# Kernel tuning notes

Hardware: AMD Instinct MI355X
Metric: run time of the kernel (lower is better)

## Reference

```python
import jax, jax.numpy as jnp
import numpy as np
from jax import lax

B, Hs, Ws = 2, 256, 256
DIM = 256        # query channels (c)
DIM_BAK = 256    # key/value channels (c2)
HEADS = 8
WIN = 8
HEAD_DIM = DIM // HEADS
SCALE = HEAD_DIM ** -0.5


def window_partition(x, ws):
    # x: [B, H, W, C] -> [B*nH*nW, ws, ws, C]
    b, h, w, c = x.shape
    x = x.reshape(b, h // ws, ws, w // ws, ws, c)
    return x.transpose(0, 1, 3, 2, 4, 5).reshape(-1, ws, ws, c)


def window_reverse(windows, ws, h, w):
    # windows: [B*nH*nW, ws, ws, C] -> [B, H, W, C]
    b = windows.shape[0] // ((h // ws) * (w // ws))
    x = windows.reshape(b, h // ws, w // ws, ws, ws, -1)
    return x.transpose(0, 1, 3, 2, 4, 5).reshape(b, h, w, -1)


def setup_inputs() -> dict:
    key = jax.random.key(0)
    ks = jax.random.split(key, 9)
    s = 0.02
    return {
        "query_feature": jax.random.normal(ks[0], (B, DIM, Hs, Ws), jnp.float32),
        "key_value_feature": jax.random.normal(ks[1], (B, DIM_BAK, Hs, Ws), jnp.float32),
        # depthwise 3x3 conv on kv (groups=DIM_BAK, bias=False): OIHW with I=1
        "w_dw": jax.random.normal(ks[2], (DIM_BAK, 1, 3, 3), jnp.float32) * s,
        # to_q: Linear(dim -> dim), stored [in, out]
        "wq": jax.random.normal(ks[3], (DIM, DIM), jnp.float32) * s,
        "bq": jax.random.normal(ks[4], (DIM,), jnp.float32) * s,
        # to_kv: Linear(dim_bak -> 2*dim)
        "wkv": jax.random.normal(ks[5], (DIM_BAK, 2 * DIM), jnp.float32) * s,
        "bkv": jax.random.normal(ks[6], (2 * DIM,), jnp.float32) * s,
        # project_out: Linear(dim -> dim)
        "w_proj": jax.random.normal(ks[7], (DIM, DIM), jnp.float32) * s,
        "b_proj": jax.random.normal(ks[8], (DIM,), jnp.float32) * s,
    }


def reference(query_feature, key_value_feature, w_dw, wq, bq, wkv, bkv, w_proj, b_proj):
    b, c, h, w = query_feature.shape
    c2 = key_value_feature.shape[1]

    # depthwise 3x3 conv on key/value feature (padding=1, stride=1)
    kv = lax.conv_general_dilated(
        key_value_feature, w_dw,
        window_strides=(1, 1), padding="SAME",
        feature_group_count=c2,
        dimension_numbers=("NCHW", "OIHW", "NCHW"))

    # NCHW -> NHWC, partition into non-overlapping windows
    qw = window_partition(query_feature.transpose(0, 2, 3, 1), WIN)  # [B_, ws, ws, c]
    kvw = window_partition(kv.transpose(0, 2, 3, 1), WIN)            # [B_, ws, ws, c2]
    B_ = qw.shape[0]
    N = WIN * WIN
    qw = qw.reshape(B_, N, c)
    kvw = kvw.reshape(B_, N, c2)

    # projections -> multi-head [B_, heads, N, head_dim]
    q = (qw @ wq + bq).reshape(B_, N, HEADS, HEAD_DIM).transpose(0, 2, 1, 3) * SCALE
    kv_proj = (kvw @ wkv + bkv).reshape(B_, N, 2, HEADS, HEAD_DIM)
    k = kv_proj[:, :, 0].transpose(0, 2, 1, 3)
    v = kv_proj[:, :, 1].transpose(0, 2, 1, 3)

    # windowed cross-attention
    attn = jax.nn.softmax(jnp.einsum("bhnd,bhmd->bhnm", q, k), axis=-1)
    out = jnp.einsum("bhnm,bhmd->bhnd", attn, v)
    out = out.transpose(0, 2, 1, 3).reshape(B_, N, c)
    out = out @ w_proj + b_proj

    # reverse windows, back to NCHW
    out = window_reverse(out.reshape(B_, WIN, WIN, c), WIN, h, w)
    return out.transpose(0, 3, 1, 2)
```

## Files before the change

kernel.cpp:

```cpp
#include <hip/hip_runtime.h>
#include <hip/hip_bf16.h>
#include <cstdint>
#include <cstddef>

typedef __hip_bfloat16 bf16;
typedef short bf16x8 __attribute__((ext_vector_type(8)));
typedef float f32x4 __attribute__((ext_vector_type(4)));

#define MFMA(a, b, c) __builtin_amdgcn_mfma_f32_16x16x32_bf16((a), (b), (c), 0, 0, 0)

__global__ __launch_bounds__(256) void stage_k(
    const float* __restrict__ wq, const float* __restrict__ wkv,
    const float* __restrict__ wp, bf16* __restrict__ wqT,
    bf16* __restrict__ wkvT, bf16* __restrict__ wpT,
    const float* __restrict__ qf, bf16* __restrict__ qwM,
    const float* __restrict__ kvf, bf16* __restrict__ SK,
    int b0, int nb, int skmask, int wbP, int do_w) {
  __shared__ bf16 T[64][66];
  int bid = blockIdx.x;
  int tid = threadIdx.x;
  int wb = do_w ? 1024 : 0;
  if (bid < wb) {
    int idx = bid * 256 + tid;
    if (idx < 65536) {
      int n = idx >> 8, k = idx & 255;
      wqT[idx] = __float2bfloat16(wq[k * 256 + n]);
    } else if (idx < 196608) {
      int i = idx - 65536;
      int n = i >> 8, k = i & 255;
      wkvT[i] = __float2bfloat16(wkv[k * 512 + n]);
    } else {
      int i = idx - 196608;
      int n = i >> 8, k = i & 255;
      wpT[i] = __float2bfloat16(wp[k * 256 + n]);
    }
    return;
  }
  int tile = bid - wb;
  int qtiles = nb * 4096;
  if (tile < qtiles) {
    int b = b0 + (tile >> 12);
    int t = tile & 4095;
    int c0 = (t & 3) << 6;
    int hwb = (t >> 2) << 6;
    const float* src = qf + ((size_t)b << 24);
    {
      int hwl = tid & 63, cb = tid >> 6;
      const float* s = src + (size_t)(c0 + cb) * 65536 + hwb + hwl;
#pragma unroll
      for (int i = 0; i < 16; ++i)
        T[cb + i * 4][hwl] = __float2bfloat16(s[(size_t)i * 4 * 65536]);
    }
    __syncthreads();
    {
      int cl = tid & 63, hb = tid >> 6;
      int swoff = b * 1024 - wbP;
#pragma unroll
      for (int j = 0; j < 16; ++j) {
        int hwl = hb + j * 4;
        int hw = hwb + hwl;
        int h = hw >> 8, w = hw & 255;
        int sw = swoff + ((h >> 3) << 5) + (w >> 3);
        int tt = ((h & 7) << 3) + (w & 7);
        qwM[((size_t)(sw * 64 + tt) << 8) + c0 + cl] = T[cl][hwl];
      }
    }
  } else {
    tile -= qtiles;
    int b = b0 + (tile >> 12);
    int t = tile & 4095;
    int c0 = (t & 3) << 6;
    int hwoff = (t >> 2) << 6;
    const float* src = kvf + ((size_t)b << 24);
    bf16* dst = SK + (size_t)(b & skmask) * 16777216;
    {
      int hwl = tid & 63, cb = tid >> 6;
      const float* s = src + (size_t)(c0 + cb) * 65536 + hwoff + hwl;
#pragma unroll
      for (int i = 0; i < 16; ++i)
        T[cb + i * 4][hwl] = __float2bfloat16(s[(size_t)i * 4 * 65536]);
    }
    __syncthreads();
    {
      int cl = tid & 63, hb = tid >> 6;
#pragma unroll
      for (int j = 0; j < 16; ++j) {
        int hwl = hb + j * 4;
        dst[((size_t)(hwoff + hwl) << 8) + c0 + cl] = T[cl][hwl];
      }
    }
  }
}

__global__ __launch_bounds__(256) void wtrans_k(const float* __restrict__ wq,
                                                const float* __restrict__ wkv,
                                                const float* __restrict__ wp,
                                                bf16* __restrict__ wqT,
                                                bf16* __restrict__ wkvT,
                                                bf16* __restrict__ wpT) {
  int idx = blockIdx.x * 256 + threadIdx.x;
  if (idx < 65536) {
    int n = idx >> 8, k = idx & 255;
    wqT[idx] = __float2bfloat16(wq[k * 256 + n]);
  } else if (idx < 196608) {
    int i = idx - 65536;
    int n = i >> 8, k = i & 255;
    wkvT[i] = __float2bfloat16(wkv[k * 512 + n]);
  } else {
    int i = idx - 196608;
    int n = i >> 8, k = i & 255;
    wpT[i] = __float2bfloat16(wp[k * 256 + n]);
  }
}

__global__ __launch_bounds__(256) void t_winq_k(const float* __restrict__ src,
                                                bf16* __restrict__ dst,
                                                int hw0, int swoff) {
  __shared__ bf16 T[64][66];
  int tile = blockIdx.x;
  int c0 = (tile & 3) << 6;
  int hwb = hw0 + ((tile >> 2) << 6);
  int tid = threadIdx.x;
  {
    int hwl = tid & 63, cb = tid >> 6;
    const float* s = src + (size_t)(c0 + cb) * 65536 + hwb + hwl;
#pragma unroll
    for (int i = 0; i < 16; ++i)
      T[cb + i * 4][hwl] = __float2bfloat16(s[(size_t)i * 4 * 65536]);
  }
  __syncthreads();
  {
    int cl = tid & 63, hb = tid >> 6;
#pragma unroll
    for (int j = 0; j < 16; ++j) {
      int hwl = hb + j * 4;
      int hw = hwb + hwl;
      int h = hw >> 8, w = hw & 255;
      int sw = swoff + ((h >> 3) << 5) + (w >> 3);
      int t = ((h & 7) << 3) + (w & 7);
      dst[((size_t)(sw * 64 + t) << 8) + c0 + cl] = T[cl][hwl];
    }
  }
}

__global__ __launch_bounds__(256) void t_nhwc_k(const float* __restrict__ src,
                                                bf16* __restrict__ dst) {
  __shared__ bf16 T[64][66];
  int tile = blockIdx.x;
  int c0 = (tile & 3) << 6;
  int hwoff = (tile >> 2) << 6;
  int tid = threadIdx.x;
  {
    int hwl = tid & 63, cb = tid >> 6;
    const float* s = src + (size_t)(c0 + cb) * 65536 + hwoff + hwl;
#pragma unroll
    for (int i = 0; i < 16; ++i)
      T[cb + i * 4][hwl] = __float2bfloat16(s[(size_t)i * 4 * 65536]);
  }
  __syncthreads();
  {
    int cl = tid & 63, hb = tid >> 6;
#pragma unroll
    for (int j = 0; j < 16; ++j) {
      int hwl = hb + j * 4;
      dst[((size_t)(hwoff + hwl) << 8) + c0 + cl] = T[cl][hwl];
    }
  }
}

__global__ __launch_bounds__(256) void convkv_k(const bf16* __restrict__ SK,
                                                const float* __restrict__ wdw,
                                                const bf16* __restrict__ wkvT,
                                                const float* __restrict__ bkv,
                                                bf16* __restrict__ k_s,
                                                bf16* __restrict__ vT_s,
                                                int wid_base, int cnt, int psw0,
                                                int skmask) {
  __shared__ __align__(16) bf16 X[64 * 256];
  auto xp = [&](int row, int col) -> bf16* {
    int by = (row << 9) + (col << 1);
    by ^= (row & 7) << 4;
    return (bf16*)((char*)X + by);
  };
  int bid = blockIdx.x;
  int swc = (bid & 7) * (cnt >> 3) + (bid >> 3);
  int sw = psw0 + swc;
  int wid = wid_base + swc;
  int b = wid >> 10;
  int rem = wid & 1023, wh = rem >> 5, ww = rem & 31;
  int h0 = wh * 8, w0 = ww * 8;
  const bf16* SKb = SK + (size_t)(b & skmask) * 16777216;
  int tid = threadIdx.x;
  {
    int tg = tid >> 7;
    int cg = tid & 127;
    float wr0[9], wr1[9];
#pragma unroll
    for (int q = 0; q < 9; ++q) {
      wr0[q] = wdw[(cg * 2) * 9 + q];
      wr1[q] = wdw[(cg * 2 + 1) * 9 + q];
    }
    const bool wlo = (w0 > 0), whi = (w0 < 248);
    float rows[3][10][2];
    auto load_row = [&](int gh, float (*r)[2]) {
      if (gh >= 0 && gh < 256) {
        const bf16* rp = SKb + ((size_t)(gh * 256 + w0) << 8) + cg * 2;
        auto up = [&](int off, float* d) {
          uint32_t v = *(const uint32_t*)&rp[off];
          d[0] = __uint_as_float(v << 16);
          d[1] = __uint_as_float(v & 0xffff0000u);
        };
        if (wlo) up(-256, r[0]); else { r[0][0] = 0.f; r[0][1] = 0.f; }
#pragma unroll
        for (int s = 1; s <= 8; ++s) up((s - 1) * 256, r[s]);
        if (whi) up(8 * 256, r[9]); else { r[9][0] = 0.f; r[9][1] = 0.f; }
      } else {
#pragma unroll
        for (int e = 0; e < 10; ++e) { r[e][0] = 0.f; r[e][1] = 0.f; }
      }
    };
    int hb = h0 + tg * 4;
    load_row(hb - 1, rows[0]);
    load_row(hb, rows[1]);
#pragma unroll
    for (int ir = 0; ir < 4; ++ir) {
      load_row(hb + ir + 1, rows[(ir + 2) % 3]);
#pragma unroll
      for (int j = 0; j < 8; ++j) {
        float a0 = 0.f, a1 = 0.f;
#pragma unroll
        for (int di = 0; di < 3; ++di) {
          const float(*rp)[2] = rows[(ir + di) % 3];
#pragma unroll
          for (int dj = 0; dj < 3; ++dj) {
            a0 = __builtin_fmaf(wr0[di * 3 + dj], rp[j + dj][0], a0);
            a1 = __builtin_fmaf(wr1[di * 3 + dj], rp[j + dj][1], a1);
          }
        }
        bf16* p = xp((tg * 4 + ir) * 8 + j, cg * 2);
        p[0] = __float2bfloat16(a0);
        p[1] = __float2bfloat16(a1);
      }
    }
  }
  __syncthreads();
  int wave = tid >> 6, lane = tid & 63, quad = lane >> 4, l16 = lane & 15;
  int n0 = wave * 64;
  f32x4 zero4 = {0.f, 0.f, 0.f, 0.f};
  f32x4 acc[4][4];
  for (int mt = 0; mt < 4; ++mt)
    for (int nt = 0; nt < 4; ++nt) acc[mt][nt] = zero4;
  for (int k0 = 0; k0 < 256; k0 += 32) {
    bf16x8 a[4], bb[4];
    for (int mt = 0; mt < 4; ++mt)
      a[mt] = *(const bf16x8*)xp(mt * 16 + l16, k0 + quad * 8);
    for (int nt = 0; nt < 4; ++nt)
      bb[nt] = *(const bf16x8*)&wkvT[(size_t)(n0 + nt * 16 + l16) * 256 + k0 + quad * 8];
    for (int mt = 0; mt < 4; ++mt)
      for (int nt = 0; nt < 4; ++nt) acc[mt][nt] = MFMA(a[mt], bb[nt], acc[mt][nt]);
  }
  for (int nt = 0; nt < 4; ++nt) {
    int n = n0 + nt * 16 + l16;
    float bias = bkv[n];
    for (int mt = 0; mt < 4; ++mt) {
      int mb = mt * 16 + quad * 4;
      for (int r = 0; r < 4; ++r)
        k_s[((size_t)(sw * 64 + mb + r) << 8) + n] =
            __float2bfloat16(acc[mt][nt][r] + bias);
    }
  }
  for (int mt = 0; mt < 4; ++mt)
    for (int nt = 0; nt < 4; ++nt) acc[mt][nt] = zero4;
  for (int k0 = 0; k0 < 256; k0 += 32) {
    bf16x8 a[4], bb[4];
    for (int mt = 0; mt < 4; ++mt)
      a[mt] = *(const bf16x8*)xp(mt * 16 + l16, k0 + quad * 8);
    for (int nt = 0; nt < 4; ++nt)
      bb[nt] = *(const bf16x8*)&wkvT[(size_t)(256 + n0 + nt * 16 + l16) * 256 + k0 + quad * 8];
    for (int mt = 0; mt < 4; ++mt)
      for (int nt = 0; nt < 4; ++nt) acc[mt][nt] = MFMA(bb[nt], a[mt], acc[mt][nt]);
  }
  for (int nt = 0; nt < 4; ++nt) {
    for (int r = 0; r < 4; ++r) {
      int vd = n0 + nt * 16 + quad * 4 + r;
      float bias = bkv[256 + vd];
      for (int mt = 0; mt < 4; ++mt)
        vT_s[((size_t)(sw * 256 + vd) << 6) + mt * 16 + l16] =
            __float2bfloat16(acc[mt][nt][r] + bias);
    }
  }
}

__global__ __launch_bounds__(256, 2) void fused_k(const bf16* __restrict__ qwM,
                                                  const bf16* __restrict__ wqT,
                                                  const float* __restrict__ bq,
                                                  const bf16* __restrict__ k_s,
                                                  const bf16* __restrict__ vT_s,
                                                  const bf16* __restrict__ wpT,
                                                  const float* __restrict__ bp,
                                                  float* __restrict__ out,
                                                  int wid_base, int nw) {
  __shared__ __align__(16) bf16 XQ[64 * 256];
  int bid = blockIdx.x;
  int sw = (bid & 7) * (nw >> 3) + (bid >> 3);
  int wid = wid_base + sw;
  int b = wid >> 10, rem = wid & 1023, wh = rem >> 5, ww = rem & 31;
  int h0 = wh * 8, w0 = ww * 8;
  int tid = threadIdx.x, wave = tid >> 6, lane = tid & 63, quad = lane >> 4, l16 = lane & 15;
  const bf16* kw = k_s + ((size_t)sw << 14);
  const bf16* vw = vT_s + ((size_t)sw << 14);

  {
    const char* Aq = (const char*)(qwM + ((size_t)sw << 14));
#pragma unroll
    for (int rr = 0; rr < 8; ++rr) {
      int L = rr * 4096 + wave * 1024 + lane * 16;
      int gl = L ^ (((L >> 9) & 7) << 4);
      __builtin_amdgcn_global_load_lds(
          (const __attribute__((address_space(1))) void*)(Aq + gl),
          (__attribute__((address_space(3))) void*)((char*)XQ + rr * 4096 + wave * 1024),
          16, 0, 0);
    }
  }
  bf16x8 kfr[2][4], vfr[2][2][2];
#pragma unroll
  for (int hi = 0; hi < 2; ++hi) {
    int co = (wave + hi * 4) * 32;
#pragma unroll
    for (int nt = 0; nt < 4; ++nt)
      kfr[hi][nt] = *(const bf16x8*)&kw[(size_t)(nt * 16 + l16) * 256 + co + quad * 8];
#pragma unroll
    for (int half = 0; half < 2; ++half)
#pragma unroll
      for (int nt = 0; nt < 2; ++nt)
        vfr[hi][half][nt] =
            *(const bf16x8*)&vw[(size_t)(co + nt * 16 + l16) * 64 + half * 32 + quad * 8];
  }
  __syncthreads();

  auto xq = [&](int row, int col) -> const bf16* {
    int by = (row << 9) + (col << 1);
    by ^= (row & 7) << 4;
    return (const bf16*)((const char*)XQ + by);
  };
  char* Abase = (char*)XQ + wave * 8192;
  auto ap = [&](int row, int col) -> bf16* {
    int by = (row << 7) + (col << 1);
    by ^= (row & 7) << 4;
    return (bf16*)(Abase + by);
  };
  auto apR = [&](int w, int row, int col) -> bf16* {
    int by = (row << 7) + (col << 1);
    by ^= (row & 7) << 4;
    return (bf16*)((char*)XQ + w * 8192 + by);
  };
  f32x4 zero4 = {0.f, 0.f, 0.f, 0.f};

  f32x4 qacc[4][4];
  for (int mt = 0; mt < 4; ++mt)
    for (int nt = 0; nt < 4; ++nt) qacc[mt][nt] = zero4;
  for (int k0 = 0; k0 < 256; k0 += 32) {
    bf16x8 a[4], bb[4];
    for (int mt = 0; mt < 4; ++mt)
      a[mt] = *(const bf16x8*)xq(mt * 16 + l16, k0 + quad * 8);
    for (int nt = 0; nt < 4; ++nt) {
      int n = (wave + ((nt >> 1) << 2)) * 32 + (nt & 1) * 16 + l16;
      bb[nt] = *(const bf16x8*)&wqT[(size_t)n * 256 + k0 + quad * 8];
    }
    for (int mt = 0; mt < 4; ++mt)
      for (int nt = 0; nt < 4; ++nt) qacc[mt][nt] = MFMA(a[mt], bb[nt], qacc[mt][nt]);
  }
  __syncthreads();
  {
    const float scale = 0.1767766952966369f;
    for (int nt = 0; nt < 4; ++nt) {
      int n = (wave + ((nt >> 1) << 2)) * 32 + (nt & 1) * 16 + l16;
      float bias = bq[n];
      for (int mt = 0; mt < 4; ++mt) {
        int mb = mt * 16 + quad * 4;
        for (int r = 0; r < 4; ++r)
          *ap(mb + r, nt * 16 + l16) =
              __float2bfloat16((qacc[mt][nt][r] + bias) * scale);
      }
    }
  }
#pragma unroll
  for (int hi = 0; hi < 2; ++hi) {
    int lc = hi * 32;
    f32x4 s[4][4];
    for (int mt = 0; mt < 4; ++mt)
      for (int nt = 0; nt < 4; ++nt) s[mt][nt] = zero4;
    {
      bf16x8 a[4];
      for (int mt = 0; mt < 4; ++mt)
        a[mt] = *(const bf16x8*)ap(mt * 16 + l16, lc + quad * 8);
      __builtin_amdgcn_s_setprio(1);
      for (int mt = 0; mt < 4; ++mt)
#pragma unroll
        for (int nt = 0; nt < 4; ++nt) s[mt][nt] = MFMA(a[mt], kfr[hi][nt], s[mt][nt]);
      __builtin_amdgcn_s_setprio(0);
    }
    float rsum[4][4];
    for (int mt = 0; mt < 4; ++mt) {
      for (int r = 0; r < 4; ++r) {
        float m = s[mt][0][r];
        for (int nt = 1; nt < 4; ++nt) m = fmaxf(m, s[mt][nt][r]);
        m = fmaxf(m, __shfl_xor(m, 1, 64));
        m = fmaxf(m, __shfl_xor(m, 2, 64));
        m = fmaxf(m, __shfl_xor(m, 4, 64));
        m = fmaxf(m, __shfl_xor(m, 8, 64));
        float sum = 0.f;
        for (int nt = 0; nt < 4; ++nt) {
          float e = __expf(s[mt][nt][r] - m);
          s[mt][nt][r] = e;
          sum += e;
        }
        sum += __shfl_xor(sum, 1, 64);
        sum += __shfl_xor(sum, 2, 64);
        sum += __shfl_xor(sum, 4, 64);
        sum += __shfl_xor(sum, 8, 64);
        rsum[mt][r] = sum;
      }
    }
    f32x4 o[4][2];
    for (int mt = 0; mt < 4; ++mt)
      for (int nt = 0; nt < 2; ++nt) o[mt][nt] = zero4;
#pragma unroll
    for (int half = 0; half < 2; ++half) {
      for (int mt = 0; mt < 4; ++mt)
#pragma unroll
        for (int nt2 = 0; nt2 < 2; ++nt2)
          for (int r = 0; r < 4; ++r)
            *ap(mt * 16 + quad * 4 + r, lc + nt2 * 16 + l16) =
                __float2bfloat16(s[mt][half * 2 + nt2][r]);
      bf16x8 pa[4];
      for (int mt = 0; mt < 4; ++mt)
        pa[mt] = *(const bf16x8*)ap(mt * 16 + l16, lc + quad * 8);
      __builtin_amdgcn_s_setprio(1);
      for (int mt = 0; mt < 4; ++mt)
#pragma unroll
        for (int nt = 0; nt < 2; ++nt)
          o[mt][nt] = MFMA(pa[mt], vfr[hi][half][nt], o[mt][nt]);
      __builtin_amdgcn_s_setprio(0);
    }
    for (int mt = 0; mt < 4; ++mt) {
      int mb = mt * 16 + quad * 4;
      for (int nt = 0; nt < 2; ++nt)
        for (int r = 0; r < 4; ++r)
          *ap(mb + r, lc + nt * 16 + l16) =
              __float2bfloat16(o[mt][nt][r] / rsum[mt][r]);
    }
  }
  __syncthreads();
  {
    int n0 = wave * 64;
    f32x4 acc[4][4];
    for (int mt = 0; mt < 4; ++mt)
      for (int nt = 0; nt < 4; ++nt) acc[mt][nt] = zero4;
    for (int k0 = 0; k0 < 256; k0 += 32) {
      int head = k0 >> 5;
      int rw = head & 3;
      int lc = (head >> 2) * 32;
      bf16x8 a[4], bb[4];
      for (int mt = 0; mt < 4; ++mt)
        a[mt] = *(const bf16x8*)apR(rw, mt * 16 + l16, lc + quad * 8);
      for (int nt = 0; nt < 4; ++nt)
        bb[nt] = *(const bf16x8*)&wpT[(size_t)(n0 + nt * 16 + l16) * 256 + k0 + quad * 8];
      for (int mt = 0; mt < 4; ++mt)
        for (int nt = 0; nt < 4; ++nt) acc[mt][nt] = MFMA(a[mt], bb[nt], acc[mt][nt]);
    }
    for (int nt = 0; nt < 4; ++nt) {
      int n = n0 + nt * 16 + l16;
      float bias = bp[n];
      float* chan = out + ((size_t)(b * 256 + n) << 16);
      for (int mt = 0; mt < 4; ++mt) {
        int row_i = mt * 2 + (quad >> 1);
        int j0 = (quad & 1) * 4;
        f32x4 v4;
        for (int r = 0; r < 4; ++r) v4[r] = acc[mt][nt][r] + bias;
        *(f32x4*)&chan[(size_t)(h0 + row_i) * 256 + w0 + j0] = v4;
      }
    }
  }
}

extern "C" void kernel_launch(void* const* d_in, const int* in_sizes, int n_in,
                              void* d_out, int out_size, void* d_ws, size_t ws_size,
                              hipStream_t stream) {
  const float* qf  = (const float*)d_in[0];
  const float* kvf = (const float*)d_in[1];
  const float* wdw = (const float*)d_in[2];
  const float* wq  = (const float*)d_in[3];
  const float* bq  = (const float*)d_in[4];
  const float* wkv = (const float*)d_in[5];
  const float* bkv = (const float*)d_in[6];
  const float* wp  = (const float*)d_in[7];
  const float* bp  = (const float*)d_in[8];
  float* out = (float*)d_out;

  bf16* wqT  = (bf16*)d_ws;
  bf16* wkvT = wqT + 65536;
  bf16* wpT  = wkvT + 131072;
  bf16* bufs = wpT + 65536;
  const size_t welems = 65536 + 131072 + 65536;
  const size_t skel = (size_t)256 * 256 * 256;

  size_t fitelems = welems + 2 * skel + (size_t)3 * 2048 * 16384;
  if (fitelems * 2 <= ws_size) {
    bf16* SK  = bufs;
    bf16* qwM = SK + 2 * skel;
    bf16* KS  = qwM + (size_t)2048 * 16384;
    bf16* VT  = KS + (size_t)2048 * 16384;
    stage_k<<<1024 + 2 * 4096 * 2, 256, 0, stream>>>(
        wq, wkv, wp, wqT, wkvT, wpT, qf, qwM, kvf, SK,
        0, 2, 1, 0, 1);
    convkv_k<<<2048, 256, 0, stream>>>(SK, wdw, wkvT, bkv, KS, VT,
                                       0, 2048,
                                       0, 1);
    fused_k<<<2048, 256, 0, stream>>>(qwM, wqT, bq, KS, VT, wpT, bp, out,
                                      0, 2048);
    return;
  }

  size_t midelems = welems + skel + (size_t)3 * 1024 * 16384;
  if (midelems * 2 <= ws_size) {
    bf16* SK  = bufs;
    bf16* qwM = SK + skel;
    bf16* KS  = qwM + (size_t)1024 * 16384;
    bf16* VT  = KS + (size_t)1024 * 16384;
    wtrans_k<<<1024, 256, 0, stream>>>(wq, wkv, wp, wqT, wkvT, wpT);
    for (int b = 0; b < 2; ++b) {
      stage_k<<<2 * 4096, 256, 0, stream>>>(
          wq, wkv, wp, wqT, wkvT, wpT, qf, qwM, kvf, SK,
          b, 1, 0, b * 1024, 0);
      convkv_k<<<1024, 256, 0, stream>>>(SK, wdw, wkvT, bkv, KS, VT,
                                         b * 1024, 1024, 0, 0);
      fused_k<<<1024, 256, 0, stream>>>(qwM, wqT, bq, KS, VT, wpT, bp, out,
                                        b * 1024, 1024);
    }
    return;
  }

  int passes = 4;
  while (passes < 32 &&
         (welems + skel + (size_t)3 * (2048 / passes) * 16384) * 2 > ws_size)
    passes <<= 1;
  int nw = 2048 / passes;
  size_t sz = (size_t)nw * 16384;
  bf16* SK  = bufs;
  bf16* qwM = SK + skel;
  bf16* KS  = qwM + sz;
  bf16* VT  = KS + sz;
  wtrans_k<<<1024, 256, 0, stream>>>(wq, wkv, wp, wqT, wkvT, wpT);
  for (int p = 0; p < passes; ++p) {
    int wbP = p * nw;
    int b0 = wbP >> 10, b1 = (wbP + nw - 1) >> 10;
    for (int b = b0; b <= b1; ++b) {
      int s = wbP > b * 1024 ? wbP : b * 1024;
      int e = (wbP + nw) < (b + 1) * 1024 ? (wbP + nw) : (b + 1) * 1024;
      int cnt = e - s;
      int h0 = ((s & 1023) >> 5) * 8;
      t_winq_k<<<cnt * 4, 256, 0, stream>>>(qf + ((size_t)b << 24), qwM,
                                            h0 * 256, b * 1024 - wbP);
      t_nhwc_k<<<4096, 256, 0, stream>>>(kvf + ((size_t)b << 24), SK);
      convkv_k<<<cnt, 256, 0, stream>>>(SK, wdw, wkvT, bkv, KS, VT,
                                        s, cnt, s - wbP, 0);
    }
    fused_k<<<nw, 256, 0, stream>>>(qwM, wqT, bq, KS, VT, wpT, bp, out, wbP, nw);
  }
}
```

Measured before the change: 573.2 us.

## Stage key/value per batch through a single reused NHWC buffer

```diff
diff --git a/kernel.cpp b/kernel.cpp
--- a/kernel.cpp
+++ b/kernel.cpp
@@ -9,13 +9,13 @@
 
 #define MFMA(a, b, c) __builtin_amdgcn_mfma_f32_16x16x32_bf16((a), (b), (c), 0, 0, 0)
 
-__global__ __launch_bounds__(256) void stage_k(
+__global__ __launch_bounds__(256) void stage2_k(
+    int do_w, int nq, int qb0, int nkv, int kvb0, int wbP,
     const float* __restrict__ wq, const float* __restrict__ wkv,
     const float* __restrict__ wp, bf16* __restrict__ wqT,
     bf16* __restrict__ wkvT, bf16* __restrict__ wpT,
     const float* __restrict__ qf, bf16* __restrict__ qwM,
-    const float* __restrict__ kvf, bf16* __restrict__ SK,
-    int b0, int nb, int skmask, int wbP, int do_w) {
+    const float* __restrict__ kvf, bf16* __restrict__ SK) {
   __shared__ bf16 T[64][66];
   int bid = blockIdx.x;
   int tid = threadIdx.x;
@@ -37,9 +37,9 @@
     return;
   }
   int tile = bid - wb;
-  int qtiles = nb * 4096;
+  int qtiles = nq * 4096;
   if (tile < qtiles) {
-    int b = b0 + (tile >> 12);
+    int b = qb0 + (tile >> 12);
     int t = tile & 4095;
     int c0 = (t & 3) << 6;
     int hwb = (t >> 2) << 6;
@@ -67,12 +67,11 @@
     }
   } else {
     tile -= qtiles;
-    int b = b0 + (tile >> 12);
+    int b = kvb0 + (tile >> 12);
     int t = tile & 4095;
     int c0 = (t & 3) << 6;
     int hwoff = (t >> 2) << 6;
     const float* src = kvf + ((size_t)b << 24);
-    bf16* dst = SK + (size_t)(b & skmask) * 16777216;
     {
       int hwl = tid & 63, cb = tid >> 6;
       const float* s = src + (size_t)(c0 + cb) * 65536 + hwoff + hwl;
@@ -86,7 +85,7 @@
 #pragma unroll
       for (int j = 0; j < 16; ++j) {
         int hwl = hb + j * 4;
-        dst[((size_t)(hwoff + hwl) << 8) + c0 + cl] = T[cl][hwl];
+        SK[((size_t)(hwoff + hwl) << 8) + c0 + cl] = T[cl][hwl];
       }
     }
   }
@@ -174,8 +173,7 @@
                                                 const float* __restrict__ bkv,
                                                 bf16* __restrict__ k_s,
                                                 bf16* __restrict__ vT_s,
-                                                int wid_base, int cnt, int psw0,
-                                                int skmask) {
+                                                int wid_base, int cnt, int psw0) {
   __shared__ __align__(16) bf16 X[64 * 256];
   auto xp = [&](int row, int col) -> bf16* {
     int by = (row << 9) + (col << 1);
@@ -186,10 +184,8 @@
   int swc = (bid & 7) * (cnt >> 3) + (bid >> 3);
   int sw = psw0 + swc;
   int wid = wid_base + swc;
-  int b = wid >> 10;
   int rem = wid & 1023, wh = rem >> 5, ww = rem & 31;
   int h0 = wh * 8, w0 = ww * 8;
-  const bf16* SKb = SK + (size_t)(b & skmask) * 16777216;
   int tid = threadIdx.x;
   {
     int tg = tid >> 7;
@@ -204,7 +200,7 @@
     float rows[3][10][2];
     auto load_row = [&](int gh, float (*r)[2]) {
       if (gh >= 0 && gh < 256) {
-        const bf16* rp = SKb + ((size_t)(gh * 256 + w0) << 8) + cg * 2;
+        const bf16* rp = SK + ((size_t)(gh * 256 + w0) << 8) + cg * 2;
         auto up = [&](int off, float* d) {
           uint32_t v = *(const uint32_t*)&rp[off];
           d[0] = __uint_as_float(v << 16);
@@ -505,20 +501,21 @@
   const size_t welems = 65536 + 131072 + 65536;
   const size_t skel = (size_t)256 * 256 * 256;
 
-  size_t fitelems = welems + 2 * skel + (size_t)3 * 2048 * 16384;
+  size_t fitelems = welems + skel + (size_t)3 * 2048 * 16384;
   if (fitelems * 2 <= ws_size) {
     bf16* SK  = bufs;
-    bf16* qwM = SK + 2 * skel;
+    bf16* qwM = SK + skel;
     bf16* KS  = qwM + (size_t)2048 * 16384;
     bf16* VT  = KS + (size_t)2048 * 16384;
-    stage_k<<<1024 + 2 * 4096 * 2, 256, 0, stream>>>(
-        wq, wkv, wp, wqT, wkvT, wpT, qf, qwM, kvf, SK,
-        0, 2, 1, 0, 1);
-    convkv_k<<<2048, 256, 0, stream>>>(SK, wdw, wkvT, bkv, KS, VT,
-                                       0, 2048,
-                                       0, 1);
-    fused_k<<<2048, 256, 0, stream>>>(qwM, wqT, bq, KS, VT, wpT, bp, out,
-                                      0, 2048);
+    stage2_k<<<1024 + 2 * 4096 + 4096, 256, 0, stream>>>(
+        1, 2, 0, 1, 0, 0, wq, wkv, wp, wqT, wkvT, wpT, qf, qwM, kvf, SK);
+    convkv_k<<<1024, 256, 0, stream>>>(SK, wdw, wkvT, bkv, KS, VT, 0, 1024, 0);
+    stage2_k<<<4096, 256, 0, stream>>>(
+        0, 0, 0, 1, 1, 0, wq, wkv, wp, wqT, wkvT, wpT, qf, qwM, kvf, SK);
+    convkv_k<<<1024, 256, 0, stream>>>(SK, wdw, wkvT, bkv, KS, VT, 1024, 1024,
+                                       1024);
+    fused_k<<<2048, 256, 0, stream>>>(qwM, wqT, bq, KS, VT, wpT, bp, out, 0,
+                                      2048);
     return;
   }
 
@@ -528,13 +525,12 @@
     bf16* qwM = SK + skel;
     bf16* KS  = qwM + (size_t)1024 * 16384;
     bf16* VT  = KS + (size_t)1024 * 16384;
-    wtrans_k<<<1024, 256, 0, stream>>>(wq, wkv, wp, wqT, wkvT, wpT);
     for (int b = 0; b < 2; ++b) {
-      stage_k<<<2 * 4096, 256, 0, stream>>>(
-          wq, wkv, wp, wqT, wkvT, wpT, qf, qwM, kvf, SK,
-          b, 1, 0, b * 1024, 0);
-      convkv_k<<<1024, 256, 0, stream>>>(SK, wdw, wkvT, bkv, KS, VT,
-                                         b * 1024, 1024, 0, 0);
+      stage2_k<<<(b == 0 ? 1024 : 0) + 4096 + 4096, 256, 0, stream>>>(
+          b == 0 ? 1 : 0, 1, b, 1, b, b * 1024, wq, wkv, wp, wqT, wkvT, wpT,
+          qf, qwM, kvf, SK);
+      convkv_k<<<1024, 256, 0, stream>>>(SK, wdw, wkvT, bkv, KS, VT, b * 1024,
+                                         1024, 0);
       fused_k<<<1024, 256, 0, stream>>>(qwM, wqT, bq, KS, VT, wpT, bp, out,
                                         b * 1024, 1024);
     }
@@ -563,8 +559,8 @@
       t_winq_k<<<cnt * 4, 256, 0, stream>>>(qf + ((size_t)b << 24), qwM,
                                             h0 * 256, b * 1024 - wbP);
       t_nhwc_k<<<4096, 256, 0, stream>>>(kvf + ((size_t)b << 24), SK);
-      convkv_k<<<cnt, 256, 0, stream>>>(SK, wdw, wkvT, bkv, KS, VT,
-                                        s, cnt, s - wbP, 0);
+      convkv_k<<<cnt, 256, 0, stream>>>(SK, wdw, wkvT, bkv, KS, VT, s, cnt,
+                                        s - wbP);
     }
     fused_k<<<nw, 256, 0, stream>>>(qwM, wqT, bq, KS, VT, wpT, bp, out, wbP, nw);
   }
```

Measured after the change: 579.7 us. About the same (+1.1%).
